# Optimization experiments

Hardware: AMD Instinct MI355X
Metric: run time of the kernel (lower is better)

## Reference

```python
import jax, jax.numpy as jnp
import numpy as np
from jax import lax

B, T = 64, 1000
DEC, ENC, ATT, FILT, KS = 1024, 512, 128, 32, 31
PAD = (KS - 1) // 2


def setup_inputs() -> dict:
    key = jax.random.key(0)
    ks = jax.random.split(key, 9)
    return {
        "decoder_hidden": jax.random.normal(ks[0], (B, DEC), dtype=jnp.float32),
        "encoder_outputs": jax.random.normal(ks[1], (B, T, ENC), dtype=jnp.float32),
        "prev_weights": jax.random.uniform(ks[2], (B, T), dtype=jnp.float32),
        "prev_weights_cum": jax.random.uniform(ks[3], (B, T), dtype=jnp.float32),
        "mask": jnp.zeros((B, T), dtype=bool),
        # learned parameters (torch Linear weight layout: [out, in])
        "conv_w": jax.random.normal(ks[4], (FILT, 2, KS), dtype=jnp.float32) * 0.05,
        "loc_proj_w": jax.random.normal(ks[5], (ATT, FILT), dtype=jnp.float32) * 0.05,
        "query_w": jax.random.normal(ks[6], (ATT, DEC), dtype=jnp.float32) * 0.02,
        "key_w": jax.random.normal(ks[7], (ATT, ENC), dtype=jnp.float32) * 0.02,
        "value_w": jax.random.normal(ks[8], (1, ATT), dtype=jnp.float32) * 0.05,
    }


def reference(decoder_hidden, encoder_outputs, prev_weights, prev_weights_cum,
              mask, conv_w, loc_proj_w, query_w, key_w, value_w):
    # query: (B, ATT)
    query = decoder_hidden @ query_w.T
    # keys: (B, T, ATT)
    keys = jnp.einsum('bte,ae->bta', encoder_outputs, key_w)
    # location features: (B, 2, T) -> conv -> (B, FILT, T)
    loc_feats = jnp.stack([prev_weights, prev_weights_cum], axis=1)
    proc_loc = lax.conv_general_dilated(
        loc_feats, conv_w, window_strides=(1,), padding=[(PAD, PAD)],
        dimension_numbers=('NCH', 'OIH', 'NCH'))
    # (B, T, FILT) -> (B, T, ATT)
    proc_loc = jnp.einsum('bft,af->bta', proc_loc, loc_proj_w)
    # energies: (B, T)
    hidden = jnp.tanh(query[:, None, :] + keys + proc_loc)
    energies = jnp.einsum('bta,a->bt', hidden, value_w[0])
    energies = jnp.where(mask, -jnp.inf, energies)
    attention_weights = jax.nn.softmax(energies, axis=1)
    # context: (B, ENC)
    context = jnp.einsum('bt,bte->be', attention_weights, encoder_outputs)
    return context, attention_weights
```

## Files before the change

kernel.cpp:

```cpp
#include <hip/hip_runtime.h>
#include <hip/hip_bf16.h>
#include <math.h>

#define BB   64
#define TT   1000
#define DEC  1024
#define ENCD 512
#define ATT  128
#define FILT 32
#define KSZ  31
#define PADW 15
#define BT   64
#define KC   64
#define XWN  96

typedef __attribute__((ext_vector_type(8))) short bf16x8;
typedef __attribute__((ext_vector_type(4))) float f32x4;

static __device__ __forceinline__ ushort f2bf(float f) {
    union { float f; unsigned u; } v; v.f = f;
    unsigned r = (v.u + 0x7FFFu + ((v.u >> 16) & 1u)) >> 16;
    return (ushort)r;
}

static __device__ __forceinline__ bf16x8 cvt8(float4 lo, float4 hi) {
    union { __hip_bfloat162 h[4]; bf16x8 v; } u;
    u.h[0] = __float22bfloat162_rn(make_float2(lo.x, lo.y));
    u.h[1] = __float22bfloat162_rn(make_float2(lo.z, lo.w));
    u.h[2] = __float22bfloat162_rn(make_float2(hi.x, hi.y));
    u.h[3] = __float22bfloat162_rn(make_float2(hi.z, hi.w));
    return u.v;
}

static __device__ __forceinline__ float fast_tanh(float x) {
    float e = __expf(2.f * x);
    return 1.f - 2.f * __builtin_amdgcn_rcpf(e + 1.f);
}

static __device__ __forceinline__ void gl2lds16(const void* g, void* l) {
    __builtin_amdgcn_global_load_lds(
        (const __attribute__((address_space(1))) unsigned*)g,
        (__attribute__((address_space(3))) unsigned*)l, 16, 0, 0);
}

__global__ __launch_bounds__(256) void k_prep(const float* __restrict__ kw,
                                              const float* __restrict__ cw,
                                              const float* __restrict__ lpw,
                                              const float* __restrict__ dh,
                                              const float* __restrict__ qw,
                                              const float* __restrict__ vw,
                                              ushort* __restrict__ kwbF,
                                              float* __restrict__ q,
                                              float* __restrict__ Mbuf) {
    __shared__ float qred[128];
    if (blockIdx.x < 32) {
        int idx = blockIdx.x * 256 + threadIdx.x;
        int l  = idx & 63;
        int n  = (idx >> 6) & 7;
        int ks = (idx >> 9) & 1;
        int c  = idx >> 10;
        int a  = n * 16 + (l & 15);
        int k0 = c * 64 + ks * 32 + (l >> 4) * 8;
        ushort u[8];
        #pragma unroll
        for (int j = 0; j < 8; ++j) u[j] = f2bf(kw[a * ENCD + k0 + j]);
        *(uint4*)&kwbF[(size_t)idx * 8] = *(const uint4*)u;
    } else if (blockIdx.x < 36) {
        int idx = (blockIdx.x - 32) * 256 + threadIdx.x;
        int l  = idx & 63;
        int n  = (idx >> 6) & 7;
        int ks = (idx >> 9) & 1;
        int a  = n * 16 + (l & 15);
        int s  = l >> 4;
        ushort u[8];
        #pragma unroll
        for (int j = 0; j < 8; ++j) {
            int k = s * 8 + j;
            float v = 0.f;
            if (k < KSZ) {
                #pragma unroll
                for (int f = 0; f < FILT; ++f)
                    v += cw[(f * 2 + ks) * KSZ + k] * lpw[a * FILT + f];
            }
            u[j] = f2bf(v);
        }
        *(uint4*)&kwbF[(size_t)(((16 + ks) * 8 + n) * 64 + l) * 8] = *(const uint4*)u;
    } else if (blockIdx.x == 36) {
        if (threadIdx.x < 64) {
            float m0 = fabsf(vw[threadIdx.x]) + fabsf(vw[threadIdx.x + 64]);
            #pragma unroll
            for (int off = 1; off < 64; off <<= 1) m0 += __shfl_xor(m0, off, 64);
            if (threadIdx.x == 0) Mbuf[0] = m0;
        }
    } else {
        int b  = blockIdx.x - 37;
        int a  = threadIdx.x & 127;
        int kh = threadIdx.x >> 7;
        const float* dhb = dh + b * DEC + kh * 512;
        const float* qwa = qw + a * DEC + kh * 512;
        float s = 0.f;
        #pragma unroll 4
        for (int k = 0; k < 512; k += 4) {
            float4 x = *(const float4*)&dhb[k];
            float4 w = *(const float4*)&qwa[k];
            s += x.x * w.x + x.y * w.y + x.z * w.z + x.w * w.w;
        }
        if (kh == 1) qred[a] = s;
        __syncthreads();
        if (kh == 0) q[b * ATT + a] = s + qred[a];
    }
}

__global__ __launch_bounds__(256) void k_energies(
    const float* __restrict__ enc, const float* __restrict__ pw,
    const float* __restrict__ pwc, const unsigned char* __restrict__ mask,
    const ushort* __restrict__ kwbF, const float* __restrict__ vw,
    const float* __restrict__ q, const float* __restrict__ Mbuf,
    float* __restrict__ expE, float* __restrict__ pctx,
    float* __restrict__ ps)
{
    __shared__ __align__(16) float Ab[2][BT * 64];
    __shared__ __align__(16) float xw[2][XWN];
    __shared__ float pequad[4][BT];
    __shared__ float sExp[BT];

    const int swz  = (blockIdx.x & 7) * 128 + (blockIdx.x >> 3);
    const int b    = swz >> 4;
    const int tile = swz & 15;
    const int t0   = tile * BT;
    const int tid  = threadIdx.x;
    const int w    = tid >> 6;
    const int l    = tid & 63;
    const int r    = l & 15;
    const int sl   = l >> 4;

    const float* encb = enc + (size_t)b * TT * ENCD;

    const int c4src = (l & 15) ^ (w * 4 + (l >> 4));
    const float* aSrc[4];
    #pragma unroll
    for (int j = 0; j < 4; ++j) {
        int rw  = (j * 4 + w) * 4 + (l >> 4);
        int tg  = t0 + rw; if (tg >= TT) tg = TT - 1;
        aSrc[j] = encb + (size_t)tg * ENCD + c4src * 4;
    }

    for (int i = tid; i < 2 * XWN; i += 256) {
        int c  = i / XWN;
        int ii = i - c * XWN;
        int tg = t0 + ii - PADW;
        const float* src = c ? pwc : pw;
        xw[c][ii] = (ii < BT + KSZ - 1 && tg >= 0 && tg < TT) ? src[b * TT + tg] : 0.f;
    }

    uint4 bfr0[2][2], bfr1[2][2];
    auto loadB = [&](uint4 (&dst)[2][2], int c) {
        #pragma unroll
        for (int ks = 0; ks < 2; ++ks)
            #pragma unroll
            for (int nn = 0; nn < 2; ++nn)
                dst[ks][nn] = *(const uint4*)&kwbF[(size_t)(((c * 2 + ks) * 8 + w * 2 + nn) * 64 + l) * 8];
    };
    auto issueA = [&](int c, int buf) {
        #pragma unroll
        for (int j = 0; j < 4; ++j)
            gl2lds16(aSrc[j] + c * KC, (char*)Ab[buf] + (j * 4 + w) * 1024);
    };

    f32x4 acc[4][2];
    #pragma unroll
    for (int i = 0; i < 4; ++i)
        #pragma unroll
        for (int n = 0; n < 2; ++n) acc[i][n] = (f32x4){0.f, 0.f, 0.f, 0.f};

    auto compute = [&](int c, const uint4 (&bfr)[2][2]) {
        __builtin_amdgcn_s_setprio(1);
        #pragma unroll
        for (int ks = 0; ks < 2; ++ks) {
            const int s2 = 2 * (ks * 4 + sl);
            bf16x8 af[4];
            #pragma unroll
            for (int i = 0; i < 4; ++i) {
                int row = i * 16 + r;
                if (c < 8) {
                    const char* base = (const char*)Ab[c & 1] + row * 256;
                    float4 alo = *(const float4*)(base + ((s2 ^ r) << 4));
                    float4 ahi = *(const float4*)(base + (((s2 | 1) ^ r) << 4));
                    af[i] = cvt8(alo, ahi);
                } else {
                    const float* xp = &xw[ks][row + sl * 8];
                    float4 alo = make_float4(xp[0], xp[1], xp[2], xp[3]);
                    float4 ahi = make_float4(xp[4], xp[5], xp[6], xp[7]);
                    af[i] = cvt8(alo, ahi);
                }
            }
            #pragma unroll
            for (int i = 0; i < 4; ++i)
                #pragma unroll
                for (int nn = 0; nn < 2; ++nn)
                    acc[i][nn] = __builtin_amdgcn_mfma_f32_16x16x32_bf16(
                        af[i], *(const bf16x8*)&bfr[ks][nn], acc[i][nn], 0, 0, 0);
        }
        __builtin_amdgcn_s_setprio(0);
    };

    issueA(0, 0); loadB(bfr0, 0);
    issueA(1, 1); loadB(bfr1, 1);
    asm volatile("s_waitcnt vmcnt(8) lgkmcnt(0)" ::: "memory");
    __builtin_amdgcn_sched_barrier(0);
    __builtin_amdgcn_s_barrier();

    #pragma unroll
    for (int c = 0; c < 9; ++c) {
        if (c & 1) compute(c, bfr1); else compute(c, bfr0);
        if (c == 8) break;
        __builtin_amdgcn_s_barrier();
        __builtin_amdgcn_sched_barrier(0);
        if (c + 2 <= 8) {
            if (c + 2 <= 7) issueA(c + 2, c & 1);
            if (c & 1) loadB(bfr1, c + 2); else loadB(bfr0, c + 2);
        }
        if (c <= 5)      asm volatile("s_waitcnt vmcnt(8)" ::: "memory");
        else if (c == 6) asm volatile("s_waitcnt vmcnt(4)" ::: "memory");
        else             asm volatile("s_waitcnt vmcnt(0)" ::: "memory");
        __builtin_amdgcn_sched_barrier(0);
        __builtin_amdgcn_s_barrier();
    }

    const float* qb = q + b * ATT;
    const float M = Mbuf[0];
    float pe[4][4];
    #pragma unroll
    for (int i = 0; i < 4; ++i)
        #pragma unroll
        for (int rr = 0; rr < 4; ++rr) pe[i][rr] = 0.f;
    #pragma unroll
    for (int nn = 0; nn < 2; ++nn) {
        int a = w * 32 + nn * 16 + r;
        float vvn = vw[a];
        float qvn = qb[a];
        #pragma unroll
        for (int i = 0; i < 4; ++i)
            #pragma unroll
            for (int rr = 0; rr < 4; ++rr)
                pe[i][rr] += vvn * fast_tanh(acc[i][nn][rr] + qvn);
    }
    #pragma unroll
    for (int m = 1; m < 16; m <<= 1)
        #pragma unroll
        for (int i = 0; i < 4; ++i)
            #pragma unroll
            for (int rr = 0; rr < 4; ++rr)
                pe[i][rr] += __shfl_xor(pe[i][rr], m, 64);
    if (r == 0) {
        #pragma unroll
        for (int i = 0; i < 4; ++i)
            #pragma unroll
            for (int rr = 0; rr < 4; ++rr)
                pequad[w][i * 16 + sl * 4 + rr] = pe[i][rr];
    }
    __syncthreads();
    if (tid < BT) {
        int t = t0 + tid;
        float e = pequad[0][tid] + pequad[1][tid] + pequad[2][tid] + pequad[3][tid];
        float v = 0.f;
        if (t < TT && !mask[b * TT + t]) v = __expf(e - M);
        if (t < TT) expE[b * TT + t] = v;
        sExp[tid] = v;
        float sv = v;
        #pragma unroll
        for (int off = 1; off < 64; off <<= 1) sv += __shfl_xor(sv, off, 64);
        if (tid == 0) ps[b * 16 + tile] = sv;
    }
    __syncthreads();

    const int tmax = (TT - t0 < BT) ? (TT - t0) : BT;
    float2 cacc = make_float2(0.f, 0.f);
    const float* pbase = encb + (size_t)t0 * ENCD + tid * 2;
    for (int t = 0; t < tmax; ++t) {
        float s = sExp[t];
        float2 v = *(const float2*)(pbase + (size_t)t * ENCD);
        cacc.x += s * v.x; cacc.y += s * v.y;
    }
    *(float2*)&pctx[(size_t)(b * 16 + tile) * ENCD + tid * 2] = cacc;
}

__global__ __launch_bounds__(512) void k_ctx_reduce(const float* __restrict__ pctx,
                                                    const float* __restrict__ ps,
                                                    const float* __restrict__ expE,
                                                    float* __restrict__ ctx,
                                                    float* __restrict__ wout) {
    int b = blockIdx.x, tid = threadIdx.x;
    __shared__ float sps[16];
    if (tid < 16) sps[tid] = ps[b * 16 + tid];
    __syncthreads();
    float s = 0.f;
    #pragma unroll
    for (int i = 0; i < 16; ++i) s += sps[i];
    float inv = 1.f / s;
    float a = 0.f;
    #pragma unroll
    for (int i = 0; i < 16; ++i) a += pctx[(size_t)(b * 16 + i) * ENCD + tid];
    ctx[b * ENCD + tid] = a * inv;
    for (int t = tid; t < TT; t += 512)
        wout[b * TT + t] = expE[b * TT + t] * inv;
}

extern "C" void kernel_launch(void* const* d_in, const int* in_sizes, int n_in,
                              void* d_out, int out_size, void* d_ws, size_t ws_size,
                              hipStream_t stream) {
    const float* dh   = (const float*)d_in[0];
    const float* enc  = (const float*)d_in[1];
    const float* pw   = (const float*)d_in[2];
    const float* pwc  = (const float*)d_in[3];
    const unsigned char* mask = (const unsigned char*)d_in[4];
    const float* cw   = (const float*)d_in[5];
    const float* lpw  = (const float*)d_in[6];
    const float* qw   = (const float*)d_in[7];
    const float* kw   = (const float*)d_in[8];
    const float* vw   = (const float*)d_in[9];

    float* out_ctx = (float*)d_out;
    float* out_w   = out_ctx + BB * ENCD;

    float* wsf    = (float*)d_ws;
    float*  q     = wsf;
    float*  expE  = wsf + 8192;
    float*  ps    = wsf + 8192 + 64000;
    float*  pctx  = wsf + 8192 + 64000 + 1024;
    ushort* kwbF  = (ushort*)(wsf + 8192 + 64000 + 1024 + 524288);
    float*  Mbuf  = wsf + 8192 + 64000 + 1024 + 524288 + 36864;

    k_prep    <<<dim3(101),  dim3(256), 0, stream>>>(kw, cw, lpw, dh, qw, vw, kwbF, q, Mbuf);
    k_energies<<<dim3(1024), dim3(256), 0, stream>>>(enc, pw, pwc, mask, kwbF, vw, q, Mbuf, expE, pctx, ps);
    k_ctx_reduce <<<dim3(BB), dim3(512), 0, stream>>>(pctx, ps, expE, out_ctx, out_w);
}
```

Before: 70.55 us.

## Stage encoder tiles through registers and store bf16 in LDS

Replaces the direct global-to-LDS fp32 loads of encoder tiles with register-staged loads that convert to bf16 before writing a swizzled bf16 tile to LDS. This halves the LDS footprint and LDS read traffic per MFMA fragment and removes the per-compute fp32-to-bf16 conversion. The B operand now uses a single register buffer loaded one chunk ahead instead of two chunks ahead, and the setprio hints are dropped. The exchange is extra VGPR use and conversion work in the write path, plus global-load latency that register staging may now expose.

```diff
diff --git a/kernel.cpp b/kernel.cpp
--- a/kernel.cpp
+++ b/kernel.cpp
@@ -35,12 +35,6 @@
 static __device__ __forceinline__ float fast_tanh(float x) {
     float e = __expf(2.f * x);
     return 1.f - 2.f * __builtin_amdgcn_rcpf(e + 1.f);
-}
-
-static __device__ __forceinline__ void gl2lds16(const void* g, void* l) {
-    __builtin_amdgcn_global_load_lds(
-        (const __attribute__((address_space(1))) unsigned*)g,
-        (__attribute__((address_space(3))) unsigned*)l, 16, 0, 0);
 }
 
 __global__ __launch_bounds__(256) void k_prep(const float* __restrict__ kw,
@@ -119,7 +113,7 @@
     float* __restrict__ expE, float* __restrict__ pctx,
     float* __restrict__ ps)
 {
-    __shared__ __align__(16) float Ab[2][BT * 64];
+    __shared__ __align__(16) ushort Ab[2][BT * KC];
     __shared__ __align__(16) float xw[2][XWN];
     __shared__ float pequad[4][BT];
     __shared__ float sExp[BT];
@@ -136,14 +130,70 @@
 
     const float* encb = enc + (size_t)b * TT * ENCD;
 
-    const int c4src = (l & 15) ^ (w * 4 + (l >> 4));
-    const float* aSrc[4];
+    const int rbase = tid >> 4;
+    const int c4    = tid & 15;
+    const float* aSrcS[4];
     #pragma unroll
     for (int j = 0; j < 4; ++j) {
-        int rw  = (j * 4 + w) * 4 + (l >> 4);
-        int tg  = t0 + rw; if (tg >= TT) tg = TT - 1;
-        aSrc[j] = encb + (size_t)tg * ENCD + c4src * 4;
-    }
+        int rw = rbase + j * 16;
+        int tg = t0 + rw; if (tg >= TT) tg = TT - 1;
+        aSrcS[j] = encb + (size_t)tg * ENCD + c4 * 4;
+    }
+    const int wu  = (c4 >> 1) ^ (rbase & 7);
+    const int wof = (wu << 4) + (c4 & 1) * 8;
+
+    float4 SA[4], SB[4];
+    auto loadA = [&](float4 (&dst)[4], int c) {
+        #pragma unroll
+        for (int j = 0; j < 4; ++j) dst[j] = *(const float4*)(aSrcS[j] + c * KC);
+    };
+    auto writeA = [&](const float4 (&src)[4], int buf) {
+        #pragma unroll
+        for (int j = 0; j < 4; ++j) {
+            ushort u[4] = { f2bf(src[j].x), f2bf(src[j].y), f2bf(src[j].z), f2bf(src[j].w) };
+            *(uint2*)((char*)Ab[buf] + (rbase + j * 16) * 128 + wof) = *(const uint2*)u;
+        }
+    };
+    uint4 bfr[2][2];
+    auto loadB = [&](int c) {
+        #pragma unroll
+        for (int ks = 0; ks < 2; ++ks)
+            #pragma unroll
+            for (int nn = 0; nn < 2; ++nn)
+                bfr[ks][nn] = *(const uint4*)&kwbF[(size_t)(((c * 2 + ks) * 8 + w * 2 + nn) * 64 + l) * 8];
+    };
+
+    f32x4 acc[4][2];
+    #pragma unroll
+    for (int i = 0; i < 4; ++i)
+        #pragma unroll
+        for (int n = 0; n < 2; ++n) acc[i][n] = (f32x4){0.f, 0.f, 0.f, 0.f};
+
+    const int ru = r & 7;
+    auto compute = [&](int c) {
+        #pragma unroll
+        for (int ks = 0; ks < 2; ++ks) {
+            bf16x8 af[4];
+            #pragma unroll
+            for (int i = 0; i < 4; ++i) {
+                int row = i * 16 + r;
+                if (c < 8) {
+                    af[i] = *(const bf16x8*)((const char*)Ab[c & 1] + row * 128
+                                             + (((ks * 4 + sl) ^ ru) << 4));
+                } else {
+                    const float* xp = &xw[ks][row + sl * 8];
+                    af[i] = cvt8(make_float4(xp[0], xp[1], xp[2], xp[3]),
+                                 make_float4(xp[4], xp[5], xp[6], xp[7]));
+                }
+            }
+            #pragma unroll
+            for (int i = 0; i < 4; ++i)
+                #pragma unroll
+                for (int nn = 0; nn < 2; ++nn)
+                    acc[i][nn] = __builtin_amdgcn_mfma_f32_16x16x32_bf16(
+                        af[i], *(const bf16x8*)&bfr[ks][nn], acc[i][nn], 0, 0, 0);
+        }
+    };
 
     for (int i = tid; i < 2 * XWN; i += 256) {
         int c  = i / XWN;
@@ -153,78 +203,30 @@
         xw[c][ii] = (ii < BT + KSZ - 1 && tg >= 0 && tg < TT) ? src[b * TT + tg] : 0.f;
     }
 
-    uint4 bfr0[2][2], bfr1[2][2];
-    auto loadB = [&](uint4 (&dst)[2][2], int c) {
-        #pragma unroll
-        for (int ks = 0; ks < 2; ++ks)
-            #pragma unroll
-            for (int nn = 0; nn < 2; ++nn)
-                dst[ks][nn] = *(const uint4*)&kwbF[(size_t)(((c * 2 + ks) * 8 + w * 2 + nn) * 64 + l) * 8];
-    };
-    auto issueA = [&](int c, int buf) {
-        #pragma unroll
-        for (int j = 0; j < 4; ++j)
-            gl2lds16(aSrc[j] + c * KC, (char*)Ab[buf] + (j * 4 + w) * 1024);
-    };
-
-    f32x4 acc[4][2];
-    #pragma unroll
-    for (int i = 0; i < 4; ++i)
-        #pragma unroll
-        for (int n = 0; n < 2; ++n) acc[i][n] = (f32x4){0.f, 0.f, 0.f, 0.f};
-
-    auto compute = [&](int c, const uint4 (&bfr)[2][2]) {
-        __builtin_amdgcn_s_setprio(1);
-        #pragma unroll
-        for (int ks = 0; ks < 2; ++ks) {
-            const int s2 = 2 * (ks * 4 + sl);
-            bf16x8 af[4];
-            #pragma unroll
-            for (int i = 0; i < 4; ++i) {
-                int row = i * 16 + r;
-                if (c < 8) {
-                    const char* base = (const char*)Ab[c & 1] + row * 256;
-                    float4 alo = *(const float4*)(base + ((s2 ^ r) << 4));
-                    float4 ahi = *(const float4*)(base + (((s2 | 1) ^ r) << 4));
-                    af[i] = cvt8(alo, ahi);
-                } else {
-                    const float* xp = &xw[ks][row + sl * 8];
-                    float4 alo = make_float4(xp[0], xp[1], xp[2], xp[3]);
-                    float4 ahi = make_float4(xp[4], xp[5], xp[6], xp[7]);
-                    af[i] = cvt8(alo, ahi);
-                }
-            }
-            #pragma unroll
-            for (int i = 0; i < 4; ++i)
-                #pragma unroll
-                for (int nn = 0; nn < 2; ++nn)
-                    acc[i][nn] = __builtin_amdgcn_mfma_f32_16x16x32_bf16(
-                        af[i], *(const bf16x8*)&bfr[ks][nn], acc[i][nn], 0, 0, 0);
-        }
-        __builtin_amdgcn_s_setprio(0);
-    };
-
-    issueA(0, 0); loadB(bfr0, 0);
-    issueA(1, 1); loadB(bfr1, 1);
-    asm volatile("s_waitcnt vmcnt(8) lgkmcnt(0)" ::: "memory");
+    loadA(SA, 0); loadB(0); loadA(SB, 1);
+    writeA(SA, 0);
+    asm volatile("s_waitcnt lgkmcnt(0)" ::: "memory");
     __builtin_amdgcn_sched_barrier(0);
     __builtin_amdgcn_s_barrier();
 
     #pragma unroll
     for (int c = 0; c < 9; ++c) {
-        if (c & 1) compute(c, bfr1); else compute(c, bfr0);
+        compute(c);
         if (c == 8) break;
+        __builtin_amdgcn_sched_barrier(0);
         __builtin_amdgcn_s_barrier();
         __builtin_amdgcn_sched_barrier(0);
-        if (c + 2 <= 8) {
-            if (c + 2 <= 7) issueA(c + 2, c & 1);
-            if (c & 1) loadB(bfr1, c + 2); else loadB(bfr0, c + 2);
-        }
-        if (c <= 5)      asm volatile("s_waitcnt vmcnt(8)" ::: "memory");
-        else if (c == 6) asm volatile("s_waitcnt vmcnt(4)" ::: "memory");
-        else             asm volatile("s_waitcnt vmcnt(0)" ::: "memory");
+        loadB(c + 1);
+        if (c + 2 <= 7) {
+            if (c & 1) loadA(SB, c + 2); else loadA(SA, c + 2);
+        }
+        if (c + 1 <= 7) {
+            if (c & 1) writeA(SA, (c + 1) & 1); else writeA(SB, (c + 1) & 1);
+        }
+        asm volatile("s_waitcnt lgkmcnt(0)" ::: "memory");
         __builtin_amdgcn_sched_barrier(0);
         __builtin_amdgcn_s_barrier();
+        __builtin_amdgcn_sched_barrier(0);
     }
 
     const float* qb = q + b * ATT;
```

Result: slower. 73.82 us (+4.6%).
